# Performance work log

Hardware: AMD Instinct MI355X
Metric: run time of the kernel (lower is better)

## Reference

```python
import jax, jax.numpy as jnp
import numpy as np
import math

N_HEADS = 16
EPS = 1e-6


def rmsnorm(x, w):
    xf = x.astype(jnp.float32)
    n = xf * jax.lax.rsqrt(jnp.mean(xf * xf, axis=-1, keepdims=True) + EPS)
    return n.astype(x.dtype) * w


def setup_inputs() -> dict:
    key = jax.random.key(0)
    ks = jax.random.split(key, 8)
    B, T, C, Hf = 1, 4096, 1024, 4096
    s = lambda fan_in: 1.0 / math.sqrt(fan_in)
    return {
        "x": jax.random.normal(ks[0], (B, T, C), jnp.float32),
        "attn_norm_w": jnp.ones((C,), jnp.float32),
        "ffn_norm_w": jnp.ones((C,), jnp.float32),
        "c_attn_w": jax.random.normal(ks[1], (3 * C, C), jnp.float32) * s(C),
        "c_proj_w": jax.random.normal(ks[2], (C, C), jnp.float32) * s(C),
        "w1": jax.random.normal(ks[3], (Hf, C), jnp.float32) * s(C),
        "w2": jax.random.normal(ks[4], (C, Hf), jnp.float32) * s(Hf),
        "w3": jax.random.normal(ks[5], (Hf, C), jnp.float32) * s(C),
    }


def attention(x, c_attn_w, c_proj_w):
    B, T, C = x.shape
    hd = C // N_HEADS
    qkv = x @ c_attn_w.T  # [B,T,3C]
    q, k, v = jnp.split(qkv, 3, axis=-1)
    q = q.reshape(B, T, N_HEADS, hd).transpose(0, 2, 1, 3)  # [B,H,T,hd]
    k = k.reshape(B, T, N_HEADS, hd).transpose(0, 2, 1, 3)
    v = v.reshape(B, T, N_HEADS, hd).transpose(0, 2, 1, 3)
    att = jnp.einsum('bhqd,bhkd->bhqk', q, k) * (1.0 / math.sqrt(hd))
    mask = jnp.tril(jnp.ones((T, T), bool))  # causal
    att = jnp.where(mask, att, -jnp.inf)
    att = jax.nn.softmax(att, axis=-1)
    y = jnp.einsum('bhqk,bhkd->bhqd', att, v)
    y = y.transpose(0, 2, 1, 3).reshape(B, T, C)
    return y @ c_proj_w.T


def ffn(x, w1, w2, w3):
    return (jax.nn.silu(x @ w1.T) * (x @ w3.T)) @ w2.T


def reference(x, attn_norm_w, ffn_norm_w, c_attn_w, c_proj_w, w1, w2, w3):
    x = x + attention(rmsnorm(x, attn_norm_w), c_attn_w, c_proj_w)
    x = x + ffn(rmsnorm(x, ffn_norm_w), w1, w2, w3)
    return x
```

## Files before the change

### kernel.cpp

```cpp
#include <hip/hip_runtime.h>
#include <hip/hip_bf16.h>

typedef __hip_bfloat16 bf16;
typedef __bf16 bf16r;
typedef bf16r bf16x8 __attribute__((ext_vector_type(8)));
typedef bf16r bf16x4 __attribute__((ext_vector_type(4)));
typedef float f32x4 __attribute__((ext_vector_type(4)));

#define T_SEQ 4096
#define C_DIM 1024
#define LD_QKV 3072
#define MB(x) ((size_t)(x) << 20)

static __device__ __forceinline__ unsigned short f2bf(float f) {
    bf16 h = (bf16)f;
    return *reinterpret_cast<unsigned short*>(&h);
}

__global__ __launch_bounds__(256) void cvt_w(const float* __restrict__ src, size_t eoff,
                                             ushort4* __restrict__ dst, int n4) {
    int i = blockIdx.x * 256 + threadIdx.x;
    const int stride = gridDim.x * 256;
    const float4* s = (const float4*)(src + eoff);
    for (; i < n4; i += stride) {
        float4 v = s[i];
        ushort4 o;
        o.x = f2bf(v.x); o.y = f2bf(v.y); o.z = f2bf(v.z); o.w = f2bf(v.w);
        dst[i] = o;
    }
}

__global__ __launch_bounds__(256) void cvt_w2h(const float* __restrict__ src, int coff,
                                               ushort4* __restrict__ dst) {
    const int i = blockIdx.x * 256 + threadIdx.x;
    const int row = i >> 9;
    const int c4 = i & 511;
    float4 v = *(const float4*)(src + (size_t)row * 4096 + coff + c4 * 4);
    ushort4 o;
    o.x = f2bf(v.x); o.y = f2bf(v.y); o.z = f2bf(v.z); o.w = f2bf(v.w);
    dst[i] = o;
}

__global__ __launch_bounds__(256) void rmsnorm_k(const float* __restrict__ x,
                                                 const float* __restrict__ w,
                                                 bf16* __restrict__ out) {
    const int row = blockIdx.x;
    const int tid = threadIdx.x;
    const float* xr = x + (size_t)row * C_DIM;
    float v[4];
    float ss = 0.f;
#pragma unroll
    for (int i = 0; i < 4; i++) { v[i] = xr[tid * 4 + i]; ss += v[i] * v[i]; }
#pragma unroll
    for (int off = 32; off; off >>= 1) ss += __shfl_xor(ss, off);
    __shared__ float red[4];
    if ((tid & 63) == 0) red[tid >> 6] = ss;
    __syncthreads();
    const float tot = red[0] + red[1] + red[2] + red[3];
    const float scale = rsqrtf(tot * (1.0f / C_DIM) + 1e-6f);
#pragma unroll
    for (int i = 0; i < 4; i++) {
        const int c = tid * 4 + i;
        out[(size_t)row * C_DIM + c] = (bf16)(v[i] * scale * w[c]);
    }
}

template <int RESID, int OUTF32>
__global__ __launch_bounds__(256) void gemm128(const bf16* __restrict__ A, int lda,
                                               const bf16* __restrict__ B, int ldb,
                                               const void* __restrict__ resid,
                                               void* __restrict__ out,
                                               int N, int K) {
    __shared__ __align__(16) bf16r As[128 * 32];
    __shared__ __align__(16) bf16r Bs[128 * 32];
    const int tid = threadIdx.x;
    const int w = tid >> 6, lane = tid & 63;
    const int c = lane & 15, qd = lane >> 4;
    const int wm = w >> 1, wn = w & 1;
    const int mbase = blockIdx.y * 128;
    const int nbase = blockIdx.x * 128;

    const int srow = lane >> 2, schk = lane & 3;
    const bf16* gA = A + (size_t)(mbase + w * 32 + srow) * lda + schk * 8;
    const bf16* gB = B + (size_t)(nbase + w * 32 + srow) * ldb + schk * 8;

    f32x4 acc[4][4] = {};

    for (int k0 = 0; k0 < K; k0 += 32) {
        __syncthreads();
#pragma unroll
        for (int s = 0; s < 2; s++) {
            __builtin_amdgcn_global_load_lds(
                (const __attribute__((address_space(1))) void*)(gA + (size_t)(s * 16) * lda + k0),
                (__attribute__((address_space(3))) void*)&As[(w * 32 + s * 16) * 32], 16, 0, 0);
            __builtin_amdgcn_global_load_lds(
                (const __attribute__((address_space(1))) void*)(gB + (size_t)(s * 16) * ldb + k0),
                (__attribute__((address_space(3))) void*)&Bs[(w * 32 + s * 16) * 32], 16, 0, 0);
        }
        __syncthreads();

        bf16x8 a[4], b[4];
#pragma unroll
        for (int i = 0; i < 4; i++)
            a[i] = *(const bf16x8*)&As[(wm * 64 + i * 16 + c) * 32 + qd * 8];
#pragma unroll
        for (int j = 0; j < 4; j++)
            b[j] = *(const bf16x8*)&Bs[(wn * 64 + j * 16 + c) * 32 + qd * 8];
#pragma unroll
        for (int i = 0; i < 4; i++)
#pragma unroll
            for (int j = 0; j < 4; j++)
                acc[i][j] = __builtin_amdgcn_mfma_f32_16x16x32_bf16(a[i], b[j], acc[i][j], 0, 0, 0);
    }

#pragma unroll
    for (int i = 0; i < 4; i++) {
#pragma unroll
        for (int j = 0; j < 4; j++) {
            const int col = nbase + wn * 64 + j * 16 + c;
#pragma unroll
            for (int reg = 0; reg < 4; reg++) {
                const int row = mbase + wm * 64 + i * 16 + qd * 4 + reg;
                const size_t idx = (size_t)row * N + col;
                float v = acc[i][j][reg];
                if (RESID == 2) v += ((const float*)resid)[idx];
                if (RESID == 3) {
                    const float a1 = (float)((const bf16*)resid)[idx];
                    v = (a1 / (1.0f + __expf(-a1))) * v;
                }
                if (OUTF32)
                    ((float*)out)[idx] = v;
                else
                    ((bf16*)out)[idx] = (bf16)v;
            }
        }
    }
}

__global__ __launch_bounds__(256) void build_tr(const bf16* __restrict__ qkv,
                                                bf16* __restrict__ dst, int soff) {
    const int h = blockIdx.y;
    const int tb = blockIdx.x;
    __shared__ bf16 tile[64][65];
    const int tx = threadIdx.x & 63;
    const int ty = threadIdx.x >> 6;
    for (int rr = ty; rr < 64; rr += 4)
        tile[rr][tx] = qkv[(size_t)(tb * 64 + rr) * LD_QKV + soff + h * 64 + tx];
    __syncthreads();
    for (int rr = ty; rr < 64; rr += 4)
        dst[((size_t)h * 64 + rr) * T_SEQ + tb * 64 + tx] = tile[tx][rr];
}

__global__ __launch_bounds__(256) void attn_mfma(const bf16* __restrict__ qkv,
                                                 const bf16* __restrict__ VT,
                                                 bf16* __restrict__ y) {
    __shared__ __align__(16) bf16r Ks[128][64];
    __shared__ __align__(16) bf16r VTs[64][128];
    __shared__ __align__(16) bf16r Ps[4][16][128];

    const int w    = threadIdx.x >> 6;
    const int lane = threadIdx.x & 63;
    const int c    = lane & 15;
    const int qd   = lane >> 4;
    const int id   = blockIdx.x;
    const int h    = id & 15;
    const int qt   = id >> 4;
    const int qb   = (qt & 1) ? (63 - (qt >> 1)) : (qt >> 1);
    const int qrow = qb * 64 + w * 16 + c;
    const int sw   = c & 7;

    bf16x8 qf[2];
    {
        const bf16* qp = qkv + (size_t)qrow * LD_QKV + h * 64;
        qf[0] = *(const bf16x8*)(qp + qd * 8);
        qf[1] = *(const bf16x8*)(qp + 32 + qd * 8);
    }

    f32x4 O[4] = {};
    float m_i = -1e30f, l_i = 0.f;
    const int nkb = (qb >> 1) + 1;

    for (int kb = 0; kb < nkb; kb++) {
        __syncthreads();
#pragma unroll
        for (int ii = 0; ii < 4; ii++) {
            const int i = ii * 256 + threadIdx.x;
            const int kr = i >> 3, ch = i & 7;
            *(bf16x8*)&Ks[kr][(ch ^ (kr & 7)) * 8] =
                *(const bf16x8*)(qkv + (size_t)(kb * 128 + kr) * LD_QKV + C_DIM + h * 64 + ch * 8);
            const int vr = i >> 4, vch = i & 15;
            *(bf16x8*)&VTs[vr][(vch ^ (vr & 7)) * 8] =
                *(const bf16x8*)(VT + ((size_t)h * 64 + vr) * T_SEQ + kb * 128 + vch * 8);
        }
        __syncthreads();

        f32x4 ST[8];
#pragma unroll
        for (int kt = 0; kt < 8; kt++) {
            f32x4 z = {};
#pragma unroll
            for (int ks = 0; ks < 2; ks++) {
                bf16x8 kf = *(const bf16x8*)&Ks[kt * 16 + c][((ks * 4 + qd) ^ sw) * 8];
                z = __builtin_amdgcn_mfma_f32_16x16x32_bf16(kf, qf[ks], z, 0, 0, 0);
            }
            ST[kt] = z;
        }

        if (kb == nkb - 1) {
#pragma unroll
            for (int kt = 0; kt < 8; kt++)
#pragma unroll
                for (int r = 0; r < 4; r++) {
                    float s = ST[kt][r] * 0.125f;
                    if (kb * 128 + kt * 16 + qd * 4 + r > qrow) s = -1e30f;
                    ST[kt][r] = s;
                }
        } else {
#pragma unroll
            for (int kt = 0; kt < 8; kt++)
#pragma unroll
                for (int r = 0; r < 4; r++) ST[kt][r] *= 0.125f;
        }

        float mb = -1e30f;
#pragma unroll
        for (int kt = 0; kt < 8; kt++)
#pragma unroll
            for (int r = 0; r < 4; r++) mb = fmaxf(mb, ST[kt][r]);
        mb = fmaxf(mb, __shfl_xor(mb, 16));
        mb = fmaxf(mb, __shfl_xor(mb, 32));
        const float mnew = fmaxf(m_i, mb);
        const float alpha = __expf(m_i - mnew);
        m_i = mnew;
        float rs = 0.f;
#pragma unroll
        for (int kt = 0; kt < 8; kt++)
#pragma unroll
            for (int r = 0; r < 4; r++) {
                const float p = __expf(ST[kt][r] - mnew);
                ST[kt][r] = p;
                rs += p;
            }
        rs += __shfl_xor(rs, 16);
        rs += __shfl_xor(rs, 32);
        l_i = l_i * alpha + rs;
#pragma unroll
        for (int dt = 0; dt < 4; dt++)
#pragma unroll
            for (int r = 0; r < 4; r++) O[dt][r] *= alpha;

#pragma unroll
        for (int kt = 0; kt < 8; kt++) {
            bf16x4 pv;
#pragma unroll
            for (int r = 0; r < 4; r++) pv[r] = (bf16r)ST[kt][r];
            const int phys = (kt * 2 + (qd >> 1)) ^ sw;
            *(bf16x4*)&Ps[w][c][phys * 8 + (qd & 1) * 4] = pv;
        }

#pragma unroll
        for (int ks = 0; ks < 4; ks++) {
            bf16x8 pf = *(const bf16x8*)&Ps[w][c][((ks * 4 + qd) ^ sw) * 8];
#pragma unroll
            for (int dt = 0; dt < 4; dt++) {
                bf16x8 vf = *(const bf16x8*)&VTs[dt * 16 + c][((ks * 4 + qd) ^ sw) * 8];
                O[dt] = __builtin_amdgcn_mfma_f32_16x16x32_bf16(vf, pf, O[dt], 0, 0, 0);
            }
        }
    }

    const float inv_l = 1.0f / l_i;
#pragma unroll
    for (int dt = 0; dt < 4; dt++) {
        bf16x4 ov;
#pragma unroll
        for (int r = 0; r < 4; r++) ov[r] = (bf16r)(O[dt][r] * inv_l);
        *(bf16x4*)(y + (size_t)qrow * C_DIM + h * 64 + dt * 16 + qd * 4) = ov;
    }
}

extern "C" void kernel_launch(void* const* d_in, const int* in_sizes, int n_in,
                              void* d_out, int out_size, void* d_ws, size_t ws_size,
                              hipStream_t stream) {
    const float* x        = (const float*)d_in[0];
    const float* attn_w   = (const float*)d_in[1];
    const float* ffn_w    = (const float*)d_in[2];
    const float* c_attn_w = (const float*)d_in[3];
    const float* c_proj_w = (const float*)d_in[4];
    const float* w1       = (const float*)d_in[5];
    const float* w2       = (const float*)d_in[6];
    const float* w3       = (const float*)d_in[7];
    float* xmid = (float*)d_out;

    char* ws = (char*)d_ws;
    bf16* cwA = (bf16*)(ws);
    bf16* cwP = (bf16*)(ws + MB(6));
    bf16* rms = (bf16*)(ws + MB(8));
    bf16* qkv = (bf16*)(ws + MB(16));
    bf16* VT  = (bf16*)(ws + MB(40));
    bf16* y   = (bf16*)(ws + MB(48));
    bf16* w1h = (bf16*)(ws + MB(16));
    bf16* w3h = (bf16*)(ws + MB(20));
    bf16* w2h = (bf16*)(ws + MB(24));
    bf16* h1h = (bf16*)(ws + MB(28));

    cvt_w<<<512, 256, 0, stream>>>(c_attn_w, 0, (ushort4*)cwA, 3072 * 1024 / 4);
    cvt_w<<<512, 256, 0, stream>>>(c_proj_w, 0, (ushort4*)cwP, 1024 * 1024 / 4);
    rmsnorm_k<<<T_SEQ, 256, 0, stream>>>(x, attn_w, rms);
    gemm128<0, 0><<<dim3(24, 32), 256, 0, stream>>>(rms, C_DIM, cwA, C_DIM, nullptr, qkv, 3072, 1024);
    build_tr<<<dim3(64, 16), 256, 0, stream>>>(qkv, VT, 2 * C_DIM);
    attn_mfma<<<1024, 256, 0, stream>>>(qkv, VT, y);
    gemm128<2, 1><<<dim3(8, 32), 256, 0, stream>>>(y, C_DIM, cwP, C_DIM, x, xmid, 1024, 1024);
    rmsnorm_k<<<T_SEQ, 256, 0, stream>>>(xmid, ffn_w, rms);
    for (int hh = 0; hh < 2; hh++) {
        cvt_w<<<512, 256, 0, stream>>>(w1, (size_t)hh * 2048 * 1024, (ushort4*)w1h, 2048 * 1024 / 4);
        gemm128<0, 0><<<dim3(16, 32), 256, 0, stream>>>(rms, C_DIM, w1h, C_DIM, nullptr, h1h, 2048, 1024);
        cvt_w<<<512, 256, 0, stream>>>(w3, (size_t)hh * 2048 * 1024, (ushort4*)w3h, 2048 * 1024 / 4);
        gemm128<3, 0><<<dim3(16, 32), 256, 0, stream>>>(rms, C_DIM, w3h, C_DIM, h1h, h1h, 2048, 1024);
        cvt_w2h<<<2048, 256, 0, stream>>>(w2, hh * 2048, (ushort4*)w2h);
        gemm128<2, 1><<<dim3(8, 32), 256, 0, stream>>>(h1h, 2048, w2h, 2048, xmid, xmid, 1024, 2048);
    }
}
```

Baseline: 553.8 us.

## Keep P in registers with 16x16x16 MFMA, exp2 softmax and lazy rescaling

Removes the per-wave LDS round trip for softmax probabilities by feeding P straight from the S accumulator layout into 16x16x16 bf16 MFMAs, with the V^T LDS swizzle changed to match. The softmax now uses exp2 with log2(e) folded into the scale, and skips the running-max update and O rescale when the new block max stays within 8 of the current max. The causal block ordering is also adjusted to balance load across CUs. In exchange it issues twice as many smaller MFMAs and accepts a loosely bounded running max, which could cost some bf16 accuracy for P.

```diff
diff --git a/kernel.cpp b/kernel.cpp
--- a/kernel.cpp
+++ b/kernel.cpp
@@ -6,11 +6,13 @@
 typedef bf16r bf16x8 __attribute__((ext_vector_type(8)));
 typedef bf16r bf16x4 __attribute__((ext_vector_type(4)));
 typedef float f32x4 __attribute__((ext_vector_type(4)));
+typedef short s16x4 __attribute__((ext_vector_type(4)));
 
 #define T_SEQ 4096
 #define C_DIM 1024
 #define LD_QKV 3072
 #define MB(x) ((size_t)(x) << 20)
+#define SCL 0.18033688011112042f
 
 static __device__ __forceinline__ unsigned short f2bf(float f) {
     bf16 h = (bf16)f;
@@ -156,7 +158,6 @@
                                                  bf16* __restrict__ y) {
     __shared__ __align__(16) bf16r Ks[128][64];
     __shared__ __align__(16) bf16r VTs[64][128];
-    __shared__ __align__(16) bf16r Ps[4][16][128];
 
     const int w    = threadIdx.x >> 6;
     const int lane = threadIdx.x & 63;
@@ -165,7 +166,8 @@
     const int id   = blockIdx.x;
     const int h    = id & 15;
     const int qt   = id >> 4;
-    const int qb   = (qt & 1) ? (63 - (qt >> 1)) : (qt >> 1);
+    const int jj   = qt >> 1;
+    const int qb   = ((qt ^ (qt >> 4)) & 1) ? (63 - jj) : jj;
     const int qrow = qb * 64 + w * 16 + c;
     const int sw   = c & 7;
 
@@ -189,7 +191,7 @@
             *(bf16x8*)&Ks[kr][(ch ^ (kr & 7)) * 8] =
                 *(const bf16x8*)(qkv + (size_t)(kb * 128 + kr) * LD_QKV + C_DIM + h * 64 + ch * 8);
             const int vr = i >> 4, vch = i & 15;
-            *(bf16x8*)&VTs[vr][(vch ^ (vr & 7)) * 8] =
+            *(bf16x8*)&VTs[vr][(vch ^ (vr & 15)) * 8] =
                 *(const bf16x8*)(VT + ((size_t)h * 64 + vr) * T_SEQ + kb * 128 + vch * 8);
         }
         __syncthreads();
@@ -211,7 +213,7 @@
             for (int kt = 0; kt < 8; kt++)
 #pragma unroll
                 for (int r = 0; r < 4; r++) {
-                    float s = ST[kt][r] * 0.125f;
+                    float s = ST[kt][r] * SCL;
                     if (kb * 128 + kt * 16 + qd * 4 + r > qrow) s = -1e30f;
                     ST[kt][r] = s;
                 }
@@ -219,7 +221,7 @@
 #pragma unroll
             for (int kt = 0; kt < 8; kt++)
 #pragma unroll
-                for (int r = 0; r < 4; r++) ST[kt][r] *= 0.125f;
+                for (int r = 0; r < 4; r++) ST[kt][r] *= SCL;
         }
 
         float mb = -1e30f;
@@ -229,42 +231,50 @@
             for (int r = 0; r < 4; r++) mb = fmaxf(mb, ST[kt][r]);
         mb = fmaxf(mb, __shfl_xor(mb, 16));
         mb = fmaxf(mb, __shfl_xor(mb, 32));
-        const float mnew = fmaxf(m_i, mb);
-        const float alpha = __expf(m_i - mnew);
-        m_i = mnew;
+
+        bf16x4 pv[8];
         float rs = 0.f;
-#pragma unroll
-        for (int kt = 0; kt < 8; kt++)
-#pragma unroll
-            for (int r = 0; r < 4; r++) {
-                const float p = __expf(ST[kt][r] - mnew);
-                ST[kt][r] = p;
-                rs += p;
-            }
-        rs += __shfl_xor(rs, 16);
-        rs += __shfl_xor(rs, 32);
-        l_i = l_i * alpha + rs;
-#pragma unroll
-        for (int dt = 0; dt < 4; dt++)
-#pragma unroll
-            for (int r = 0; r < 4; r++) O[dt][r] *= alpha;
+        if (__all(mb - m_i <= 8.0f)) {
+#pragma unroll
+            for (int kt = 0; kt < 8; kt++)
+#pragma unroll
+                for (int r = 0; r < 4; r++) {
+                    const float p = exp2f(ST[kt][r] - m_i);
+                    pv[kt][r] = (bf16r)p;
+                    rs += p;
+                }
+            rs += __shfl_xor(rs, 16);
+            rs += __shfl_xor(rs, 32);
+            l_i += rs;
+        } else {
+            const float mnew = fmaxf(m_i, mb);
+            const float alpha = exp2f(m_i - mnew);
+#pragma unroll
+            for (int kt = 0; kt < 8; kt++)
+#pragma unroll
+                for (int r = 0; r < 4; r++) {
+                    const float p = exp2f(ST[kt][r] - mnew);
+                    pv[kt][r] = (bf16r)p;
+                    rs += p;
+                }
+            rs += __shfl_xor(rs, 16);
+            rs += __shfl_xor(rs, 32);
+            l_i = l_i * alpha + rs;
+            m_i = mnew;
+#pragma unroll
+            for (int dt = 0; dt < 4; dt++)
+#pragma unroll
+                for (int r = 0; r < 4; r++) O[dt][r] *= alpha;
+        }
 
 #pragma unroll
         for (int kt = 0; kt < 8; kt++) {
-            bf16x4 pv;
-#pragma unroll
-            for (int r = 0; r < 4; r++) pv[r] = (bf16r)ST[kt][r];
-            const int phys = (kt * 2 + (qd >> 1)) ^ sw;
-            *(bf16x4*)&Ps[w][c][phys * 8 + (qd & 1) * 4] = pv;
-        }
-
-#pragma unroll
-        for (int ks = 0; ks < 4; ks++) {
-            bf16x8 pf = *(const bf16x8*)&Ps[w][c][((ks * 4 + qd) ^ sw) * 8];
+            const s16x4 pf = __builtin_bit_cast(s16x4, pv[kt]);
 #pragma unroll
             for (int dt = 0; dt < 4; dt++) {
-                bf16x8 vf = *(const bf16x8*)&VTs[dt * 16 + c][((ks * 4 + qd) ^ sw) * 8];
-                O[dt] = __builtin_amdgcn_mfma_f32_16x16x32_bf16(vf, pf, O[dt], 0, 0, 0);
+                const s16x4 vf = *(const s16x4*)&VTs[dt * 16 + c]
+                    [((kt * 2 + (qd >> 1)) ^ c) * 8 + (qd & 1) * 4];
+                O[dt] = __builtin_amdgcn_mfma_f32_16x16x16bf16_1k(vf, pf, O[dt], 0, 0, 0);
             }
         }
     }
```

Measured after the change: 632.3 us. +14.2%, slower.
